# Kernel optimization log

Measured on AMD Instinct MI355X. Metric: run time of the kernel, lower is better.

## Reference

```python
import jax, jax.numpy as jnp
import numpy as np

FRACS = (0.25, 0.5, 0.25)  # per-expert top-fraction kept, from the original forward


def setup_inputs() -> dict:
    key = jax.random.key(0)
    ks = jax.random.split(key, 10)
    B, S, D, P, E, C = 1, 65536, 1024, 512, 3, 2
    s = 0.02
    return {
        "hidden_states": jax.random.normal(ks[0], (B, S, D), jnp.float32),
        "W_t1": jax.random.normal(ks[1], (D, P), jnp.float32) * s,   # TransMIL stand-in proj
        "W_cls1": jax.random.normal(ks[2], (P, C), jnp.float32) * s, # trans1 bag classifier
        "Wg0": jax.random.normal(ks[3], (P, 2), jnp.float32) * s,    # gate
        "Wg1": jax.random.normal(ks[4], (P, 2), jnp.float32) * s,    # gate1
        "Wg2": jax.random.normal(ks[5], (P, 2), jnp.float32) * s,    # gate2
        "W_clf": jax.random.normal(ks[6], (E, P, E), jnp.float32) * s,  # per-expert classifiers
        "W_a1": jax.random.normal(ks[7], (P, P), jnp.float32) * s,   # agg1 TransMIL stand-in proj
        "W_acls": jax.random.normal(ks[8], (P, C), jnp.float32) * s, # agg1 bag classifier
    }


def reference(hidden_states, W_t1, W_cls1, Wg0, Wg1, Wg2, W_clf, W_a1, W_acls):
    B, S, D = hidden_states.shape
    x = hidden_states.reshape(-1, D)               # (T, D) tokens
    T = x.shape[0]
    # trans1 (TransMIL stand-in): per-patch feature + mean-pool bag logits
    patches = jnp.tanh(x @ W_t1)                   # (T, P) patch_feature
    bag = patches.mean(0)
    Y_logits = (bag @ W_cls1)[None, :]             # (1, C)
    Y_prob = jax.nn.softmax(Y_logits, -1)
    Y_hat = jnp.argmax(Y_logits, -1)
    # three independent routers, softmax + top-1
    router_logits = patches @ Wg0                  # (T, 2)
    rw0 = jax.nn.softmax(router_logits.astype(jnp.float32), -1)
    w_top0 = rw0.max(-1)                           # top-1 routing weight (gate0) used as sort key for ALL experts
    sel0 = jnp.argmax(rw0, -1)
    sel1 = jnp.argmax(jax.nn.softmax((patches @ Wg1).astype(jnp.float32), -1), -1)
    sel2 = jnp.argmax(jax.nn.softmax((patches @ Wg2).astype(jnp.float32), -1), -1)
    masks = [sel0 == 1, sel1 == 1, sel2 == 1]      # expert_mask[e][1] token selection
    joint_losses = jnp.float32(0.0)
    sel_fs, nums_list = [], []
    for e in range(3):
        mask = masks[e]
        cnt = mask.sum().astype(jnp.int32)
        nums = jnp.floor(cnt.astype(jnp.float32) * FRACS[e]).astype(jnp.int32)
        nums = jnp.where(nums == 0, cnt, nums)     # 'if nums != 0 else all' branch
        key_ = jnp.where(mask, w_top0, -jnp.inf)
        order = jnp.argsort(-key_)                 # descending routing weight
        rank = jnp.zeros(T, jnp.int32).at[order].set(jnp.arange(T, dtype=jnp.int32))
        sel = mask & (rank < nums)                 # top-fraction tokens of this expert
        sel_f = sel.astype(patches.dtype)
        mean_feat = (patches * sel_f[:, None]).sum(0) / jnp.maximum(nums, 1).astype(patches.dtype)
        logits = mean_feat @ W_clf[e]              # (3,)
        if e < 2:                                  # CE loss only for experts 0,1
            joint_losses = joint_losses + (-jax.nn.log_softmax(logits)[e])
        sel_fs.append(sel_f)
        nums_list.append(nums)
    # agg1 (TransMIL stand-in) over concatenated represent_patchs == multiplicity-weighted mean
    feats2 = jnp.tanh(patches @ W_a1)              # (T, P)
    total_sel = sel_fs[0] + sel_fs[1] + sel_fs[2]
    total_n = (nums_list[0] + nums_list[1] + nums_list[2]).astype(patches.dtype)
    agg_bag = (feats2 * total_sel[:, None]).sum(0) / jnp.maximum(total_n, 1.0)
    e_Y_logits = (agg_bag @ W_acls)[None, :]
    e_Y_hat = jnp.argmax(e_Y_logits, -1)
    distribute = jnp.stack([jnp.asarray(T, jnp.int32), nums_list[0], nums_list[1], nums_list[2]])
    return (e_Y_logits, e_Y_hat, Y_logits, Y_prob, Y_hat, router_logits, joint_losses, distribute)
```

## Files before the change

kernel.cpp:

```cpp
#include <hip/hip_runtime.h>
#include <cstdint>
#include <cstddef>

#define T_TOK 65536
#define DDIM  1024
#define PDIM  512

typedef __attribute__((ext_vector_type(8))) short          shortx8;
typedef __attribute__((ext_vector_type(8))) unsigned short ushortx8;
typedef __attribute__((ext_vector_type(4))) float          floatx4;

__device__ __forceinline__ unsigned short f2bf_rn(float x){
  unsigned int u = __float_as_uint(x);
  unsigned int r = u + 0x7FFFu + ((u >> 16) & 1u);
  return (unsigned short)(r >> 16);
}
__device__ __forceinline__ float bf2f(unsigned short h){
  return __uint_as_float(((unsigned int)h) << 16);
}
__device__ __forceinline__ float ftanh(float x){
  float ez = __expf(2.f * x);
  return 1.f - 2.f / (ez + 1.f);
}

__device__ __forceinline__ void gload16(const void* g, void* l){
  __builtin_amdgcn_global_load_lds(
      (const __attribute__((address_space(1))) unsigned int*)g,
      (__attribute__((address_space(3))) unsigned int*)l, 16, 0, 0);
}
__device__ __forceinline__ void bar(){
  asm volatile("" ::: "memory");
  __builtin_amdgcn_s_barrier();
  asm volatile("" ::: "memory");
}
#define WAIT_VMC(n) asm volatile("s_waitcnt vmcnt(" #n ")" ::: "memory")
#define WAIT_LGKM0  do { asm volatile("s_waitcnt lgkmcnt(0)" ::: "memory"); \
                         __builtin_amdgcn_sched_barrier(0); } while(0)

__device__ __forceinline__ void split2(const float4 a, const float4 b,
                                       ushortx8* hi, ushortx8* lo){
  float vs[8] = {a.x, a.y, a.z, a.w, b.x, b.y, b.z, b.w};
  ushortx8 h, l;
  #pragma unroll
  for (int j = 0; j < 8; j++){
    unsigned int u = __float_as_uint(vs[j]);
    float r = vs[j] - __uint_as_float(u & 0xFFFF0000u);
    h[j] = (unsigned short)(u >> 16);
    l[j] = (unsigned short)(__float_as_uint(r) >> 16);
  }
  *hi = h; *lo = l;
}


__global__ void prep(const float* __restrict__ Wt1, const float* __restrict__ Wa1,
                     unsigned short* __restrict__ W1th, unsigned short* __restrict__ W1tl,
                     unsigned short* __restrict__ Wath, unsigned short* __restrict__ Watl,
                     int* __restrict__ zbase)
{
  int gid = blockIdx.x * 256 + threadIdx.x;
  if (gid < 20544){ zbase[gid] = 0; return; }
  int i = gid - 20544;
  if (i < 524288){
    int e   = i & 7;
    int g16 = i >> 3;
    int s   = g16 & 3;
    int row = (g16 >> 2) & 255;
    int tb  = g16 >> 10;
    int nb  = tb & 1, kt = tb >> 1;
    int n = nb * 256 + row;
    int k = kt * 32 + ((s ^ ((row >> 1) & 3)) << 3) + e;
    float x = Wt1[(size_t)k * PDIM + n];
    unsigned short h = f2bf_rn(x);
    W1th[i] = h;
    W1tl[i] = f2bf_rn(x - bf2f(h));
    return;
  }
  i -= 524288;
  if (i < 262144){
    int e   = i & 7;
    int g16 = i >> 3;
    int s   = g16 & 3;
    int row = (g16 >> 2) & 255;
    int tb  = g16 >> 10;
    int nb  = tb & 1, kt = tb >> 1;
    int n = nb * 256 + row;
    int k = kt * 32 + ((s ^ ((row >> 1) & 3)) << 3) + e;
    float x = Wa1[(size_t)k * PDIM + n];
    unsigned short h = f2bf_rn(x);
    Wath[i] = h;
    Watl[i] = f2bf_rn(x - bf2f(h));
  }
}

template<int MODE>
__global__ __launch_bounds__(512, 2)
void gemm_split(const float* __restrict__ A,
                const unsigned short* __restrict__ Bhg,
                const unsigned short* __restrict__ Blg,
                float* __restrict__ Cout,
                float* __restrict__ colacc,
                const int* __restrict__ cidx,
                const float* __restrict__ wgt,
                const int* __restrict__ params)
{
  constexpr int K  = (MODE == 0) ? 1024 : 512;
  constexpr int NT = K >> 5;

  __shared__ unsigned short AhL[2][8192];
  __shared__ unsigned short AlL[2][8192];
  __shared__ unsigned short BhL[2][8192];
  __shared__ unsigned short BlL[2][8192];
  __shared__ int   cidxl[256];
  __shared__ float wl[256];

  const int tid = threadIdx.x;
  const int d = blockIdx.x + (blockIdx.y << 1);
  const int lin = (MODE == 0) ? (((d & 7) << 6) + (d >> 3)) : d;
  const int bx = lin & 1, by = lin >> 1;
  const int m0 = by << 8, n0 = bx << 8;

  if (MODE == 1){
    const int count = params[21];
    if (m0 >= count) return;
    if (tid < 256){
      int g = m0 + tid;
      if (g < count){ cidxl[tid] = cidx[g]; wl[tid] = wgt[g]; }
      else          { cidxl[tid] = 0;       wl[tid] = 0.f;   }
    }
    __syncthreads();
  }

  const int lane = tid & 63;
  const int wv   = tid >> 6;
  const int wm   = wv >> 2;
  const int wn   = wv & 3;
  const int lr   = lane & 15, quad = lane >> 4;
  const int sq   = (quad ^ ((lr >> 1) & 3)) << 4;

  const int abase = (wm * 128 + lr) * 64 + sq;
  const int bbase = (wn * 64  + lr) * 64 + sq;

  const int rowW = tid >> 1, half = tid & 1;
  const size_t arowg = (MODE == 0) ? (size_t)(m0 + rowW) : (size_t)cidxl[rowW];
  const float* ap = A + arowg * K + half * 16;
  const int rsw = (rowW >> 1) & 3;
  const int wb0 = rowW * 64 + ((( half * 2     ) ^ rsw) << 4);
  const int wb1 = rowW * 64 + ((( half * 2 + 1 ) ^ rsw) << 4);

  floatx4 acc[8][4];
  #pragma unroll
  for (int i = 0; i < 8; i++)
    #pragma unroll
    for (int j = 0; j < 4; j++)
      acc[i][j] = (floatx4){0.f, 0.f, 0.f, 0.f};

  float4 av0, av1, av2, av3;

  {
    av0 = *(const float4*)(ap + 0);
    av1 = *(const float4*)(ap + 4);
    av2 = *(const float4*)(ap + 8);
    av3 = *(const float4*)(ap + 12);
    const size_t tb = (size_t)bx * 8192;
    gload16(Bhg + tb + tid * 8,        (char*)BhL[0] + tid * 16);
    gload16(Bhg + tb + 4096 + tid * 8, (char*)BhL[0] + 8192 + tid * 16);
    gload16(Blg + tb + tid * 8,        (char*)BlL[0] + tid * 16);
    gload16(Blg + tb + 4096 + tid * 8, (char*)BlL[0] + 8192 + tid * 16);
    WAIT_VMC(4);
    ushortx8 h, l;
    split2(av0, av1, &h, &l);
    *(ushortx8*)((char*)AhL[0] + wb0) = h;
    *(ushortx8*)((char*)AlL[0] + wb0) = l;
    split2(av2, av3, &h, &l);
    *(ushortx8*)((char*)AhL[0] + wb1) = h;
    *(ushortx8*)((char*)AlL[0] + wb1) = l;
    {
      const float* apk = ap + ((NT > 1) ? 32 : 0);
      av0 = *(const float4*)(apk);
      av1 = *(const float4*)(apk + 4);
      av2 = *(const float4*)(apk + 8);
      av3 = *(const float4*)(apk + 12);
    }
    WAIT_VMC(4);
    asm volatile("s_waitcnt lgkmcnt(0)" ::: "memory");
    bar();
  }

  #pragma unroll 2
  for (int t = 0; t < NT; ++t){
    const int cur = t & 1, nxt = cur ^ 1;
    const int knB = (t + 1 < NT) ? (t + 1) : (NT - 1);
    const int knA = (t + 2 < NT) ? (t + 2) : (NT - 1);
    const char* AhC = (const char*)AhL[cur];
    const char* AlC = (const char*)AlL[cur];
    const char* BhC = (const char*)BhL[cur];
    const char* BlC = (const char*)BlL[cur];

    shortx8 aH[4], aL[4], bH0[2], bL0[2], bH1[2], bL1[2];

    #pragma unroll
    for (int mt = 0; mt < 4; mt++){
      aH[mt] = *(const shortx8*)(AhC + abase + mt * 1024);
      aL[mt] = *(const shortx8*)(AlC + abase + mt * 1024);
    }
    #pragma unroll
    for (int nt = 0; nt < 2; nt++){
      bH0[nt] = *(const shortx8*)(BhC + bbase + nt * 1024);
      bL0[nt] = *(const shortx8*)(BlC + bbase + nt * 1024);
    }
    {
      const size_t tb = (size_t)(knB * 2 + bx) * 8192;
      gload16(Bhg + tb + tid * 8,        (char*)BhL[nxt] + tid * 16);
      gload16(Bhg + tb + 4096 + tid * 8, (char*)BhL[nxt] + 8192 + tid * 16);
      gload16(Blg + tb + tid * 8,        (char*)BlL[nxt] + tid * 16);
      gload16(Blg + tb + 4096 + tid * 8, (char*)BlL[nxt] + 8192 + tid * 16);
    }
    bar();
    WAIT_LGKM0;
    __builtin_amdgcn_s_setprio(1);
    #pragma unroll
    for (int mt = 0; mt < 4; mt++)
      #pragma unroll
      for (int nt = 0; nt < 2; nt++){
        acc[mt][nt] = __builtin_amdgcn_mfma_f32_16x16x32_bf16(aH[mt], bH0[nt], acc[mt][nt], 0, 0, 0);
        acc[mt][nt] = __builtin_amdgcn_mfma_f32_16x16x32_bf16(aL[mt], bH0[nt], acc[mt][nt], 0, 0, 0);
        acc[mt][nt] = __builtin_amdgcn_mfma_f32_16x16x32_bf16(aH[mt], bL0[nt], acc[mt][nt], 0, 0, 0);
      }
    __builtin_amdgcn_s_setprio(0);
    bar();

    #pragma unroll
    for (int nt = 0; nt < 2; nt++){
      bH1[nt] = *(const shortx8*)(BhC + bbase + (2 + nt) * 1024);
      bL1[nt] = *(const shortx8*)(BlC + bbase + (2 + nt) * 1024);
    }
    WAIT_VMC(4);
    {
      ushortx8 h, l;
      split2(av0, av1, &h, &l);
      *(ushortx8*)((char*)AhL[nxt] + wb0) = h;
      *(ushortx8*)((char*)AlL[nxt] + wb0) = l;
      split2(av2, av3, &h, &l);
      *(ushortx8*)((char*)AhL[nxt] + wb1) = h;
      *(ushortx8*)((char*)AlL[nxt] + wb1) = l;
    }
    bar();
    WAIT_LGKM0;
    __builtin_amdgcn_s_setprio(1);
    #pragma unroll
    for (int mt = 0; mt < 4; mt++)
      #pragma unroll
      for (int nt = 0; nt < 2; nt++){
        acc[mt][2 + nt] = __builtin_amdgcn_mfma_f32_16x16x32_bf16(aH[mt], bH1[nt], acc[mt][2 + nt], 0, 0, 0);
        acc[mt][2 + nt] = __builtin_amdgcn_mfma_f32_16x16x32_bf16(aL[mt], bH1[nt], acc[mt][2 + nt], 0, 0, 0);
        acc[mt][2 + nt] = __builtin_amdgcn_mfma_f32_16x16x32_bf16(aH[mt], bL1[nt], acc[mt][2 + nt], 0, 0, 0);
      }
    __builtin_amdgcn_s_setprio(0);
    bar();

    #pragma unroll
    for (int mt = 0; mt < 4; mt++){
      aH[mt] = *(const shortx8*)(AhC + abase + (4 + mt) * 1024);
      aL[mt] = *(const shortx8*)(AlC + abase + (4 + mt) * 1024);
    }
    {
      const float* apk = ap + knA * 32;
      av0 = *(const float4*)(apk);
      av1 = *(const float4*)(apk + 4);
      av2 = *(const float4*)(apk + 8);
      av3 = *(const float4*)(apk + 12);
    }
    bar();
    WAIT_LGKM0;
    __builtin_amdgcn_s_setprio(1);
    #pragma unroll
    for (int mt = 0; mt < 4; mt++)
      #pragma unroll
      for (int nt = 0; nt < 2; nt++){
        acc[4 + mt][nt] = __builtin_amdgcn_mfma_f32_16x16x32_bf16(aH[mt], bH0[nt], acc[4 + mt][nt], 0, 0, 0);
        acc[4 + mt][nt] = __builtin_amdgcn_mfma_f32_16x16x32_bf16(aL[mt], bH0[nt], acc[4 + mt][nt], 0, 0, 0);
        acc[4 + mt][nt] = __builtin_amdgcn_mfma_f32_16x16x32_bf16(aH[mt], bL0[nt], acc[4 + mt][nt], 0, 0, 0);
      }
    #pragma unroll
    for (int mt = 0; mt < 4; mt++)
      #pragma unroll
      for (int nt = 0; nt < 2; nt++){
        acc[4 + mt][2 + nt] = __builtin_amdgcn_mfma_f32_16x16x32_bf16(aH[mt], bH1[nt], acc[4 + mt][2 + nt], 0, 0, 0);
        acc[4 + mt][2 + nt] = __builtin_amdgcn_mfma_f32_16x16x32_bf16(aL[mt], bH1[nt], acc[4 + mt][2 + nt], 0, 0, 0);
        acc[4 + mt][2 + nt] = __builtin_amdgcn_mfma_f32_16x16x32_bf16(aH[mt], bL1[nt], acc[4 + mt][2 + nt], 0, 0, 0);
      }
    __builtin_amdgcn_s_setprio(0);
    WAIT_VMC(4);
    bar();
  }

  float csum[4] = {0.f, 0.f, 0.f, 0.f};
  #pragma unroll
  for (int mt = 0; mt < 8; mt++){
    float w0 = 1.f, w1 = 1.f, w2 = 1.f, w3 = 1.f;
    if (MODE == 1){
      const float4 wv4 = *(const float4*)&wl[wm * 128 + mt * 16 + (quad << 2)];
      w0 = wv4.x; w1 = wv4.y; w2 = wv4.z; w3 = wv4.w;
    }
    #pragma unroll
    for (int nt = 0; nt < 4; nt++){
      float t0 = ftanh(acc[mt][nt][0]);
      float t1 = ftanh(acc[mt][nt][1]);
      float t2 = ftanh(acc[mt][nt][2]);
      float t3 = ftanh(acc[mt][nt][3]);
      if (MODE == 0){
        size_t base = (size_t)(m0 + wm * 128 + mt * 16 + (quad << 2)) * PDIM
                    + (n0 + wn * 64 + nt * 16 + lr);
        Cout[base]            = t0;
        Cout[base +     PDIM] = t1;
        Cout[base + 2 * PDIM] = t2;
        Cout[base + 3 * PDIM] = t3;
        csum[nt] += t0 + t1 + t2 + t3;
      } else {
        csum[nt] += t0 * w0 + t1 * w1 + t2 * w2 + t3 * w3;
      }
    }
  }
  #pragma unroll
  for (int nt = 0; nt < 4; nt++){
    float s = csum[nt];
    s += __shfl_xor(s, 16);
    s += __shfl_xor(s, 32);
    if (lane < 16) atomicAdd(&colacc[n0 + wn * 64 + nt * 16 + lane], s);
  }
}

__global__ void gates_kernel(const float* __restrict__ patches,
                             const float* __restrict__ Wg0,
                             const float* __restrict__ Wg1,
                             const float* __restrict__ Wg2,
                             float* __restrict__ dout,
                             unsigned int* __restrict__ wkey,
                             unsigned char* __restrict__ mask3,
                             int* __restrict__ params,
                             int* __restrict__ hist)
{
  __shared__ int lc[3];
  const int tid = threadIdx.x;
  if (tid < 3) lc[tid] = 0;
  __syncthreads();
  const int lane = tid & 63;
  float wg[3][16];
  const float* Wgp[3] = {Wg0, Wg1, Wg2};
  #pragma unroll
  for (int g = 0; g < 3; g++){
    #pragma unroll
    for (int j = 0; j < 4; j++){
      float4 v = *(const float4*)(Wgp[g] + lane * 16 + j * 4);
      wg[g][j * 4 + 0] = v.x; wg[g][j * 4 + 1] = v.y;
      wg[g][j * 4 + 2] = v.z; wg[g][j * 4 + 3] = v.w;
    }
  }
  const int nw = gridDim.x << 2;
  for (int t = blockIdx.x * 4 + (tid >> 6); t < T_TOK; t += nw){
    const float* row = patches + (size_t)t * PDIM + lane * 8;
    float4 v0 = *(const float4*)row;
    float4 v1 = *(const float4*)(row + 4);
    float x[8] = {v0.x, v0.y, v0.z, v0.w, v1.x, v1.y, v1.z, v1.w};
    float g00 = 0, g01 = 0, g10 = 0, g11 = 0, g20 = 0, g21 = 0;
    #pragma unroll
    for (int j = 0; j < 8; j++){
      g00 += x[j] * wg[0][2 * j]; g01 += x[j] * wg[0][2 * j + 1];
      g10 += x[j] * wg[1][2 * j]; g11 += x[j] * wg[1][2 * j + 1];
      g20 += x[j] * wg[2][2 * j]; g21 += x[j] * wg[2][2 * j + 1];
    }
    #pragma unroll
    for (int off = 1; off < 64; off <<= 1){
      g00 += __shfl_xor(g00, off); g01 += __shfl_xor(g01, off);
      g10 += __shfl_xor(g10, off); g11 += __shfl_xor(g11, off);
      g20 += __shfl_xor(g20, off); g21 += __shfl_xor(g21, off);
    }
    if (lane == 0){
      dout[8 + 2 * t]     = g00;
      dout[8 + 2 * t + 1] = g01;
      int m0 = g01 > g00;
      int m1 = g11 > g10;
      int m2 = g21 > g20;
      mask3[t] = (unsigned char)(m0 | (m1 << 1) | (m2 << 2));
      float d = fabsf(g00 - g01);
      float w = 1.0f / (1.0f + __expf(-d));
      unsigned int u = __float_as_uint(w);
      u = u < 0x3F000000u ? 0x3F000000u : u;
      u = u > 0x3F7FFFFFu ? 0x3F7FFFFFu : u;
      wkey[t] = u;
      int b = (int)((u >> 11) & 0xFFFu);
      if (m0){ atomicAdd(&hist[b], 1);         atomicAdd(&lc[0], 1); }
      if (m1){ atomicAdd(&hist[4096 + b], 1);  atomicAdd(&lc[1], 1); }
      if (m2){ atomicAdd(&hist[8192 + b], 1);  atomicAdd(&lc[2], 1); }
    }
  }
  __syncthreads();
  if (tid < 3 && lc[tid]) atomicAdd(&params[tid], lc[tid]);
}

__global__ void find_bucket(int* __restrict__ params, const int* __restrict__ hist)
{
  __shared__ int cs[256], orig[256];
  __shared__ int selc, selrk;
  const int tid = threadIdx.x;
  for (int e = 0; e < 3; e++){
    int cnt = params[e];
    int shift = (e == 1) ? 1 : 2;
    int nums = cnt >> shift;
    if (nums == 0) nums = cnt;
    if (tid == 0) params[3 + e] = nums;
    __syncthreads();
    if (nums == 0){
      if (tid == 0){ params[6 + e] = -1; params[9 + e] = 0; }
      __syncthreads();
      continue;
    }
    const int* h = hist + e * 4096 + tid * 16;
    int s = 0;
    #pragma unroll
    for (int j = 0; j < 16; j++) s += h[j];
    cs[tid] = s; orig[tid] = s;
    __syncthreads();
    for (int off = 1; off < 256; off <<= 1){
      int v = (tid + off < 256) ? cs[tid + off] : 0;
      __syncthreads();
      cs[tid] += v;
      __syncthreads();
    }
    if (cs[tid] >= nums && (cs[tid] - orig[tid]) < nums){
      selc = tid; selrk = nums - (cs[tid] - orig[tid]);
    }
    __syncthreads();
    if (tid == 0){
      int ch = selc, rk = selrk;
      const int* hh = hist + e * 4096 + ch * 16;
      int acc = 0;
      for (int j = 15; j >= 0; j--){
        int c = hh[j];
        if (acc + c >= rk){ params[6 + e] = ch * 16 + j; params[9 + e] = rk - acc; break; }
        acc += c;
      }
    }
    __syncthreads();
  }
}

__global__ void level2hist(const int* __restrict__ params, const unsigned int* __restrict__ wkey,
                           const unsigned char* __restrict__ mask3, int* __restrict__ h2)
{
  const int e = blockIdx.y;
  const int B = params[6 + e];
  if (B < 0) return;
  const unsigned char bit = (unsigned char)(1u << e);
  const int t0 = blockIdx.x * 2048 + threadIdx.x;
  #pragma unroll
  for (int i = 0; i < 8; i++){
    int t = t0 + i * 256;
    if (mask3[t] & bit){
      unsigned int u = wkey[t];
      if ((int)((u >> 11) & 0xFFFu) == B) atomicAdd(&h2[e * 2048 + (u & 2047u)], 1);
    }
  }
}

__global__ void find_theta(int* __restrict__ params, const int* __restrict__ h2)
{
  const int e = blockIdx.x;
  const int tid = threadIdx.x;
  __shared__ int cs[256], orig[256];
  __shared__ int selc;
  int B = params[6 + e], rank = params[9 + e];
  if (B < 0){
    if (tid == 0){ params[12 + e] = (int)0xFFFFFFFFu; params[15 + e] = 0; params[18 + e] = 0; }
    return;
  }
  const int* h = h2 + e * 2048 + tid * 8;
  int s = 0;
  #pragma unroll
  for (int j = 0; j < 8; j++) s += h[j];
  cs[tid] = s; orig[tid] = s;
  __syncthreads();
  for (int off = 1; off < 256; off <<= 1){
    int v = (tid + off < 256) ? cs[tid + off] : 0;
    __syncthreads();
    cs[tid] += v;
    __syncthreads();
  }
  if (cs[tid] >= rank && (cs[tid] - orig[tid]) < rank) selc = tid;
  __syncthreads();
  if (tid == 0){
    int ch = selc;
    int rk = rank - (cs[ch] - orig[ch]);
    const int* hh = h2 + e * 2048 + ch * 8;
    int acc = 0;
    for (int j = 7; j >= 0; j--){
      int c = hh[j];
      if (acc + c >= rk){
        int sub = ch * 8 + j;
        params[12 + e] = (int)(0x3F000000u | ((unsigned)B << 11) | (unsigned)sub);
        params[15 + e] = rk - acc;
        params[18 + e] = c;
        break;
      }
      acc += c;
    }
  }
}

__global__ void mark_sel(const int* __restrict__ params, const unsigned int* __restrict__ wkey,
                         const unsigned char* __restrict__ mask3, unsigned char* __restrict__ selb)
{
  const int e = blockIdx.y;
  const int bx = blockIdx.x;
  const int tid = threadIdx.x;
  const unsigned int theta = (unsigned int)params[12 + e];
  const int r = params[15 + e];
  const int ceq = params[18 + e];
  const unsigned char bit = (unsigned char)(1u << e);
  unsigned char* sb = selb + e * T_TOK;
  if (ceq == r){
    int t0 = bx * 2048;
    #pragma unroll
    for (int i = 0; i < 8; i++){
      int t = t0 + i * 256 + tid;
      unsigned char mk = mask3[t] & bit;
      sb[t] = (mk && wkey[t] >= theta) ? 1 : 0;
    }
  } else {
    if (bx) return;
    __shared__ int basec;
    __shared__ int wsum[4];
    if (tid == 0) basec = 0;
    __syncthreads();
    const int lane = tid & 63, w = tid >> 6;
    for (int c = 0; c < 256; c++){
      int t = c * 256 + tid;
      unsigned char mk = mask3[t] & bit;
      unsigned int u = mk ? wkey[t] : 0u;
      bool gt = mk && (u > theta);
      bool eq = mk && (u == theta);
      unsigned long long bal = __ballot(eq);
      if (lane == 0) wsum[w] = __popcll(bal);
      __syncthreads();
      int wbase = 0;
      for (int ww = 0; ww < w; ww++) wbase += wsum[ww];
      int pos = basec + wbase + __popcll(bal & ((1ull << lane) - 1ull));
      sb[t] = (gt || (eq && pos < r)) ? 1 : 0;
      __syncthreads();
      if (tid == 0) basec += wsum[0] + wsum[1] + wsum[2] + wsum[3];
      __syncthreads();
    }
  }
}

__global__ void compact(const unsigned char* __restrict__ selb, int* __restrict__ cidx,
                        float* __restrict__ wgt, int* __restrict__ params)
{
  int t = blockIdx.x * 256 + threadIdx.x;
  int ts = selb[t] + selb[T_TOK + t] + selb[2 * T_TOK + t];
  int lane = threadIdx.x & 63;
  unsigned long long bal = __ballot(ts > 0);
  int base = 0;
  if (lane == 0) base = atomicAdd(&params[21], __popcll(bal));
  base = __shfl(base, 0);
  if (ts){
    int pos = base + __popcll(bal & ((1ull << lane) - 1ull));
    cidx[pos] = t;
    wgt[pos] = (float)ts;
  }
}

__global__ void meanfeat_c(const float* __restrict__ patches, const unsigned char* __restrict__ selb,
                           const int* __restrict__ cidx, const int* __restrict__ params,
                           float* __restrict__ mf)
{
  const int count = params[21];
  const int base = blockIdx.x * 256;
  if (base >= count) return;
  const int n = min(256, count - base);
  const int tid = threadIdx.x;
  __shared__ int cl[256];
  __shared__ unsigned char f0s[256], f1s[256];
  if (tid < n){
    int c = cidx[base + tid];
    cl[tid] = c;
    f0s[tid] = selb[c];
    f1s[tid] = selb[T_TOK + c];
  }
  __syncthreads();
  float s00 = 0, s01 = 0, s10 = 0, s11 = 0;
  for (int i = 0; i < n; i++){
    int f0 = f0s[i], f1 = f1s[i];
    if (f0 | f1){
      float2 v = *(const float2*)(patches + (size_t)cl[i] * PDIM + tid * 2);
      if (f0){ s00 += v.x; s01 += v.y; }
      if (f1){ s10 += v.x; s11 += v.y; }
    }
  }
  atomicAdd(&mf[tid * 2],       s00);
  atomicAdd(&mf[tid * 2 + 1],   s01);
  atomicAdd(&mf[512 + tid * 2],     s10);
  atomicAdd(&mf[512 + tid * 2 + 1], s11);
}

__global__ void finalize(const float* __restrict__ bagsum, const float* __restrict__ aggsum,
                         const float* __restrict__ mf, const int* __restrict__ params,
                         const float* __restrict__ Wcls1, const float* __restrict__ Wclf,
                         const float* __restrict__ Wacls, float* __restrict__ dout)
{
  const int lane = threadIdx.x;
  const int nums0 = params[3], nums1 = params[4], nums2 = params[5];
  const float invT = 1.0f / 65536.0f;
  const float inv0 = 1.0f / (float)(nums0 > 0 ? nums0 : 1);
  const float inv1 = 1.0f / (float)(nums1 > 0 ? nums1 : 1);
  const float totn = (float)(nums0 + nums1 + nums2);
  const float invA = 1.0f / fmaxf(totn, 1.0f);
  float y0 = 0, y1 = 0, a0 = 0, a1 = 0;
  float l00 = 0, l01 = 0, l02 = 0, l10 = 0, l11 = 0, l12 = 0;
  #pragma unroll
  for (int j = 0; j < 8; j++){
    int p = lane * 8 + j;
    float bg = bagsum[p] * invT;
    y0 += bg * Wcls1[p * 2]; y1 += bg * Wcls1[p * 2 + 1];
    float ag = aggsum[p] * invA;
    a0 += ag * Wacls[p * 2]; a1 += ag * Wacls[p * 2 + 1];
    float m0v = mf[p] * inv0;
    l00 += m0v * Wclf[p * 3]; l01 += m0v * Wclf[p * 3 + 1]; l02 += m0v * Wclf[p * 3 + 2];
    float m1v = mf[512 + p] * inv1;
    l10 += m1v * Wclf[1536 + p * 3]; l11 += m1v * Wclf[1536 + p * 3 + 1]; l12 += m1v * Wclf[1536 + p * 3 + 2];
  }
  #pragma unroll
  for (int off = 1; off < 64; off <<= 1){
    y0 += __shfl_xor(y0, off);   y1 += __shfl_xor(y1, off);
    a0 += __shfl_xor(a0, off);   a1 += __shfl_xor(a1, off);
    l00 += __shfl_xor(l00, off); l01 += __shfl_xor(l01, off); l02 += __shfl_xor(l02, off);
    l10 += __shfl_xor(l10, off); l11 += __shfl_xor(l11, off); l12 += __shfl_xor(l12, off);
  }
  if (lane == 0){
    dout[0] = a0; dout[1] = a1;
    dout[2] = (a1 > a0) ? 1.0f : 0.0f;
    dout[3] = y0; dout[4] = y1;
    float mx = fmaxf(y0, y1), e0 = expf(y0 - mx), e1 = expf(y1 - mx), inv = 1.0f / (e0 + e1);
    dout[5] = e0 * inv; dout[6] = e1 * inv;
    dout[7] = (y1 > y0) ? 1.0f : 0.0f;
    float m3 = fmaxf(fmaxf(l00, l01), l02);
    float lse0 = m3 + logf(expf(l00 - m3) + expf(l01 - m3) + expf(l02 - m3));
    float m4 = fmaxf(fmaxf(l10, l11), l12);
    float lse1 = m4 + logf(expf(l10 - m4) + expf(l11 - m4) + expf(l12 - m4));
    dout[131080] = (lse0 - l00) + (lse1 - l11);
    dout[131081] = 65536.0f;
    dout[131082] = (float)nums0;
    dout[131083] = (float)nums1;
    dout[131084] = (float)nums2;
  }
}

extern "C" void kernel_launch(void* const* d_in, const int* in_sizes, int n_in,
                              void* d_out, int out_size, void* d_ws, size_t ws_size,
                              hipStream_t stream)
{
  const float* X      = (const float*)d_in[0];
  const float* W_t1   = (const float*)d_in[1];
  const float* W_cls1 = (const float*)d_in[2];
  const float* Wg0    = (const float*)d_in[3];
  const float* Wg1    = (const float*)d_in[4];
  const float* Wg2    = (const float*)d_in[5];
  const float* W_clf  = (const float*)d_in[6];
  const float* W_a1   = (const float*)d_in[7];
  const float* W_acls = (const float*)d_in[8];
  float* dout = (float*)d_out;
  char* ws = (char*)d_ws;

  float*          patches = (float*)         (ws + 0);
  unsigned short* W1th    = (unsigned short*)(ws + 134217728);
  unsigned short* W1tl    = (unsigned short*)(ws + 135266304);
  unsigned short* Wath    = (unsigned short*)(ws + 136314880);
  unsigned short* Watl    = (unsigned short*)(ws + 136839168);
  unsigned int*   wkey    = (unsigned int*)  (ws + 137363456);
  unsigned char*  mask3   = (unsigned char*) (ws + 137625600);
  unsigned char*  selb    = (unsigned char*) (ws + 137691136);
  int*            cidx    = (int*)           (ws + 137887744);
  float*          wgt     = (float*)         (ws + 138149888);
  int*            zbase   = (int*)           (ws + 138412032);
  int*            hist    = zbase;
  int*            h2      = zbase + 12288;
  int*            params  = zbase + 18432;
  float*          bagsum  = (float*)(zbase + 18496);
  float*          aggsum  = (float*)(zbase + 19008);
  float*          mf      = (float*)(zbase + 19520);

  prep<<<3153, 256, 0, stream>>>(W_t1, W_a1, W1th, W1tl, Wath, Watl, zbase);

  gemm_split<0><<<dim3(2, 256), 512, 0, stream>>>(
      X, W1th, W1tl, patches, bagsum, nullptr, nullptr, nullptr);

  gates_kernel<<<512, 256, 0, stream>>>(
      patches, Wg0, Wg1, Wg2, dout, wkey, mask3, params, hist);

  find_bucket<<<1, 256, 0, stream>>>(params, hist);
  level2hist<<<dim3(32, 3), 256, 0, stream>>>(params, wkey, mask3, h2);
  find_theta<<<3, 256, 0, stream>>>(params, h2);
  mark_sel<<<dim3(32, 3), 256, 0, stream>>>(params, wkey, mask3, selb);
  compact<<<256, 256, 0, stream>>>(selb, cidx, wgt, params);

  meanfeat_c<<<256, 256, 0, stream>>>(patches, selb, cidx, params, mf);

  gemm_split<1><<<dim3(2, 256), 512, 0, stream>>>(
      patches, Wath, Watl, nullptr, aggsum, cidx, wgt, params);

  finalize<<<1, 64, 0, stream>>>(bagsum, aggsum, mf, params, W_cls1, W_clf, W_acls, dout);
}
```

Baseline: 726.6 us.

## Split GEMM main loop into eight 2x2 MFMA phases with finer LDS interleaving

Restructures the inner k-loop from four large MFMA clusters into eight smaller 2x2-subtile phases, in a serpentine order that reuses A/B fragment registers across phases. LDS reads and global prefetches are interleaved between the smaller clusters. The aim is to lower register pressure and overlap LDS traffic with MFMA work. The cost is many more barriers per iteration, which may add sync overhead.

```diff
diff --git a/kernel.cpp b/kernel.cpp
--- a/kernel.cpp
+++ b/kernel.cpp
@@ -49,6 +49,23 @@
     l[j] = (unsigned short)(__float_as_uint(r) >> 16);
   }
   *hi = h; *lo = l;
+}
+
+template<int P, int Q>
+__device__ __forceinline__ void mfma12(floatx4 (&acc)[8][4],
+    const shortx8 aH[2], const shortx8 aL[2],
+    const shortx8 bH[2], const shortx8 bL[2])
+{
+  #pragma unroll
+  for (int i = 0; i < 2; i++)
+    #pragma unroll
+    for (int j = 0; j < 2; j++){
+      floatx4 c = acc[2*P+i][2*Q+j];
+      c = __builtin_amdgcn_mfma_f32_16x16x32_bf16(aH[i], bH[j], c, 0, 0, 0);
+      c = __builtin_amdgcn_mfma_f32_16x16x32_bf16(aL[i], bH[j], c, 0, 0, 0);
+      c = __builtin_amdgcn_mfma_f32_16x16x32_bf16(aH[i], bL[j], c, 0, 0, 0);
+      acc[2*P+i][2*Q+j] = c;
+    }
 }
 
 
@@ -195,74 +212,83 @@
     const char* AlC = (const char*)AlL[cur];
     const char* BhC = (const char*)BhL[cur];
     const char* BlC = (const char*)BlL[cur];
-
-    shortx8 aH[4], aL[4], bH0[2], bL0[2], bH1[2], bL1[2];
-
-    #pragma unroll
-    for (int mt = 0; mt < 4; mt++){
-      aH[mt] = *(const shortx8*)(AhC + abase + mt * 1024);
-      aL[mt] = *(const shortx8*)(AlC + abase + mt * 1024);
-    }
-    #pragma unroll
-    for (int nt = 0; nt < 2; nt++){
-      bH0[nt] = *(const shortx8*)(BhC + bbase + nt * 1024);
-      bL0[nt] = *(const shortx8*)(BlC + bbase + nt * 1024);
+    char* AhN = (char*)AhL[nxt];
+    char* AlN = (char*)AlL[nxt];
+    char* BhN = (char*)BhL[nxt];
+    char* BlN = (char*)BlL[nxt];
+
+    shortx8 aXH[2], aXL[2], aYH[2], aYL[2];
+    shortx8 b0H[2], b0L[2], b1H[2], b1L[2];
+
+    #pragma unroll
+    for (int i = 0; i < 2; i++){
+      aXH[i] = *(const shortx8*)(AhC + abase + i * 1024);
+      aXL[i] = *(const shortx8*)(AlC + abase + i * 1024);
+      b0H[i] = *(const shortx8*)(BhC + bbase + i * 1024);
+      b0L[i] = *(const shortx8*)(BlC + bbase + i * 1024);
     }
     {
       const size_t tb = (size_t)(knB * 2 + bx) * 8192;
-      gload16(Bhg + tb + tid * 8,        (char*)BhL[nxt] + tid * 16);
-      gload16(Bhg + tb + 4096 + tid * 8, (char*)BhL[nxt] + 8192 + tid * 16);
-      gload16(Blg + tb + tid * 8,        (char*)BlL[nxt] + tid * 16);
-      gload16(Blg + tb + 4096 + tid * 8, (char*)BlL[nxt] + 8192 + tid * 16);
-    }
-    bar();
-    WAIT_LGKM0;
+      gload16(Bhg + tb + tid * 8,        BhN + tid * 16);
+      gload16(Bhg + tb + 4096 + tid * 8, BhN + 8192 + tid * 16);
+      gload16(Blg + tb + tid * 8,        BlN + tid * 16);
+      gload16(Blg + tb + 4096 + tid * 8, BlN + 8192 + tid * 16);
+    }
+    bar(); WAIT_LGKM0;
     __builtin_amdgcn_s_setprio(1);
-    #pragma unroll
-    for (int mt = 0; mt < 4; mt++)
-      #pragma unroll
-      for (int nt = 0; nt < 2; nt++){
-        acc[mt][nt] = __builtin_amdgcn_mfma_f32_16x16x32_bf16(aH[mt], bH0[nt], acc[mt][nt], 0, 0, 0);
-        acc[mt][nt] = __builtin_amdgcn_mfma_f32_16x16x32_bf16(aL[mt], bH0[nt], acc[mt][nt], 0, 0, 0);
-        acc[mt][nt] = __builtin_amdgcn_mfma_f32_16x16x32_bf16(aH[mt], bL0[nt], acc[mt][nt], 0, 0, 0);
-      }
+    mfma12<0,0>(acc, aXH, aXL, b0H, b0L);
     __builtin_amdgcn_s_setprio(0);
     bar();
 
     #pragma unroll
-    for (int nt = 0; nt < 2; nt++){
-      bH1[nt] = *(const shortx8*)(BhC + bbase + (2 + nt) * 1024);
-      bL1[nt] = *(const shortx8*)(BlC + bbase + (2 + nt) * 1024);
+    for (int j = 0; j < 2; j++){
+      b1H[j] = *(const shortx8*)(BhC + bbase + (2 + j) * 1024);
+      b1L[j] = *(const shortx8*)(BlC + bbase + (2 + j) * 1024);
+    }
+    bar(); WAIT_LGKM0;
+    __builtin_amdgcn_s_setprio(1);
+    mfma12<0,1>(acc, aXH, aXL, b1H, b1L);
+    __builtin_amdgcn_s_setprio(0);
+    bar();
+
+    #pragma unroll
+    for (int i = 0; i < 2; i++){
+      aYH[i] = *(const shortx8*)(AhC + abase + (2 + i) * 1024);
+      aYL[i] = *(const shortx8*)(AlC + abase + (2 + i) * 1024);
     }
     WAIT_VMC(4);
     {
       ushortx8 h, l;
       split2(av0, av1, &h, &l);
-      *(ushortx8*)((char*)AhL[nxt] + wb0) = h;
-      *(ushortx8*)((char*)AlL[nxt] + wb0) = l;
+      *(ushortx8*)(AhN + wb0) = h;
+      *(ushortx8*)(AlN + wb0) = l;
       split2(av2, av3, &h, &l);
-      *(ushortx8*)((char*)AhL[nxt] + wb1) = h;
-      *(ushortx8*)((char*)AlL[nxt] + wb1) = l;
-    }
-    bar();
-    WAIT_LGKM0;
+      *(ushortx8*)(AhN + wb1) = h;
+      *(ushortx8*)(AlN + wb1) = l;
+    }
+    bar(); WAIT_LGKM0;
     __builtin_amdgcn_s_setprio(1);
-    #pragma unroll
-    for (int mt = 0; mt < 4; mt++)
-      #pragma unroll
-      for (int nt = 0; nt < 2; nt++){
-        acc[mt][2 + nt] = __builtin_amdgcn_mfma_f32_16x16x32_bf16(aH[mt], bH1[nt], acc[mt][2 + nt], 0, 0, 0);
-        acc[mt][2 + nt] = __builtin_amdgcn_mfma_f32_16x16x32_bf16(aL[mt], bH1[nt], acc[mt][2 + nt], 0, 0, 0);
-        acc[mt][2 + nt] = __builtin_amdgcn_mfma_f32_16x16x32_bf16(aH[mt], bL1[nt], acc[mt][2 + nt], 0, 0, 0);
-      }
+    mfma12<1,1>(acc, aYH, aYL, b1H, b1L);
     __builtin_amdgcn_s_setprio(0);
     bar();
 
-    #pragma unroll
-    for (int mt = 0; mt < 4; mt++){
-      aH[mt] = *(const shortx8*)(AhC + abase + (4 + mt) * 1024);
-      aL[mt] = *(const shortx8*)(AlC + abase + (4 + mt) * 1024);
-    }
+    bar(); WAIT_LGKM0;
+    __builtin_amdgcn_s_setprio(1);
+    mfma12<1,0>(acc, aYH, aYL, b0H, b0L);
+    __builtin_amdgcn_s_setprio(0);
+    bar();
+
+    #pragma unroll
+    for (int i = 0; i < 2; i++){
+      aXH[i] = *(const shortx8*)(AhC + abase + (4 + i) * 1024);
+      aXL[i] = *(const shortx8*)(AlC + abase + (4 + i) * 1024);
+    }
+    bar(); WAIT_LGKM0;
+    __builtin_amdgcn_s_setprio(1);
+    mfma12<2,0>(acc, aXH, aXL, b0H, b0L);
+    __builtin_amdgcn_s_setprio(0);
+    bar();
+
     {
       const float* apk = ap + knA * 32;
       av0 = *(const float4*)(apk);
@@ -270,25 +296,26 @@
       av2 = *(const float4*)(apk + 8);
       av3 = *(const float4*)(apk + 12);
     }
-    bar();
-    WAIT_LGKM0;
+    bar(); WAIT_LGKM0;
     __builtin_amdgcn_s_setprio(1);
-    #pragma unroll
-    for (int mt = 0; mt < 4; mt++)
-      #pragma unroll
-      for (int nt = 0; nt < 2; nt++){
-        acc[4 + mt][nt] = __builtin_amdgcn_mfma_f32_16x16x32_bf16(aH[mt], bH0[nt], acc[4 + mt][nt], 0, 0, 0);
-        acc[4 + mt][nt] = __builtin_amdgcn_mfma_f32_16x16x32_bf16(aL[mt], bH0[nt], acc[4 + mt][nt], 0, 0, 0);
-        acc[4 + mt][nt] = __builtin_amdgcn_mfma_f32_16x16x32_bf16(aH[mt], bL0[nt], acc[4 + mt][nt], 0, 0, 0);
-      }
-    #pragma unroll
-    for (int mt = 0; mt < 4; mt++)
-      #pragma unroll
-      for (int nt = 0; nt < 2; nt++){
-        acc[4 + mt][2 + nt] = __builtin_amdgcn_mfma_f32_16x16x32_bf16(aH[mt], bH1[nt], acc[4 + mt][2 + nt], 0, 0, 0);
-        acc[4 + mt][2 + nt] = __builtin_amdgcn_mfma_f32_16x16x32_bf16(aL[mt], bH1[nt], acc[4 + mt][2 + nt], 0, 0, 0);
-        acc[4 + mt][2 + nt] = __builtin_amdgcn_mfma_f32_16x16x32_bf16(aH[mt], bL1[nt], acc[4 + mt][2 + nt], 0, 0, 0);
-      }
+    mfma12<2,1>(acc, aXH, aXL, b1H, b1L);
+    __builtin_amdgcn_s_setprio(0);
+    bar();
+
+    #pragma unroll
+    for (int i = 0; i < 2; i++){
+      aYH[i] = *(const shortx8*)(AhC + abase + (6 + i) * 1024);
+      aYL[i] = *(const shortx8*)(AlC + abase + (6 + i) * 1024);
+    }
+    bar(); WAIT_LGKM0;
+    __builtin_amdgcn_s_setprio(1);
+    mfma12<3,1>(acc, aYH, aYL, b1H, b1L);
+    __builtin_amdgcn_s_setprio(0);
+    bar();
+
+    bar(); WAIT_LGKM0;
+    __builtin_amdgcn_s_setprio(1);
+    mfma12<3,0>(acc, aYH, aYL, b0H, b0L);
     __builtin_amdgcn_s_setprio(0);
     WAIT_VMC(4);
     bar();
```

Result: slower. 774.4 us (+6.6%).

## Shrink split-bf16 GEMM tiles from 256x256 to 128x128 with 256-thread blocks

Applied to the files above, without the earlier changes.

Reduces the gemm_split block tile from 256x256 (8 waves) to 128x128 (4 waves), halving LDS buffers and accumulator registers, and drops two of the four MFMA phases per k-step. The weight pre-swizzle in prep is changed to match the 128-wide N blocks, and the grid grows to 4x512 blocks. The aim is more resident blocks per CU and better load balance, especially for the variable-count MODE 1 pass. The cost is lower operand reuse per tile, so A and B traffic from global memory rises.

```diff
diff --git a/kernel.cpp b/kernel.cpp
--- a/kernel.cpp
+++ b/kernel.cpp
@@ -64,10 +64,10 @@
     int e   = i & 7;
     int g16 = i >> 3;
     int s   = g16 & 3;
-    int row = (g16 >> 2) & 255;
-    int tb  = g16 >> 10;
-    int nb  = tb & 1, kt = tb >> 1;
-    int n = nb * 256 + row;
+    int row = (g16 >> 2) & 127;
+    int tb  = g16 >> 9;
+    int nb  = tb & 3, kt = tb >> 2;
+    int n = nb * 128 + row;
     int k = kt * 32 + ((s ^ ((row >> 1) & 3)) << 3) + e;
     float x = Wt1[(size_t)k * PDIM + n];
     unsigned short h = f2bf_rn(x);
@@ -80,10 +80,10 @@
     int e   = i & 7;
     int g16 = i >> 3;
     int s   = g16 & 3;
-    int row = (g16 >> 2) & 255;
-    int tb  = g16 >> 10;
-    int nb  = tb & 1, kt = tb >> 1;
-    int n = nb * 256 + row;
+    int row = (g16 >> 2) & 127;
+    int tb  = g16 >> 9;
+    int nb  = tb & 3, kt = tb >> 2;
+    int n = nb * 128 + row;
     int k = kt * 32 + ((s ^ ((row >> 1) & 3)) << 3) + e;
     float x = Wa1[(size_t)k * PDIM + n];
     unsigned short h = f2bf_rn(x);
@@ -93,7 +93,7 @@
 }
 
 template<int MODE>
-__global__ __launch_bounds__(512, 2)
+__global__ __launch_bounds__(256, 2)
 void gemm_split(const float* __restrict__ A,
                 const unsigned short* __restrict__ Bhg,
                 const unsigned short* __restrict__ Blg,
@@ -106,23 +106,23 @@
   constexpr int K  = (MODE == 0) ? 1024 : 512;
   constexpr int NT = K >> 5;
 
-  __shared__ unsigned short AhL[2][8192];
-  __shared__ unsigned short AlL[2][8192];
-  __shared__ unsigned short BhL[2][8192];
-  __shared__ unsigned short BlL[2][8192];
-  __shared__ int   cidxl[256];
-  __shared__ float wl[256];
+  __shared__ unsigned short AhL[2][4096];
+  __shared__ unsigned short AlL[2][4096];
+  __shared__ unsigned short BhL[2][4096];
+  __shared__ unsigned short BlL[2][4096];
+  __shared__ int   cidxl[128];
+  __shared__ float wl[128];
 
   const int tid = threadIdx.x;
-  const int d = blockIdx.x + (blockIdx.y << 1);
-  const int lin = (MODE == 0) ? (((d & 7) << 6) + (d >> 3)) : d;
-  const int bx = lin & 1, by = lin >> 1;
-  const int m0 = by << 8, n0 = bx << 8;
+  const int d = blockIdx.x + (blockIdx.y << 2);
+  const int lin = (MODE == 0) ? (((d & 7) << 8) + (d >> 3)) : d;
+  const int bx = lin & 3, by = lin >> 2;
+  const int m0 = by << 7, n0 = bx << 7;
 
   if (MODE == 1){
     const int count = params[21];
     if (m0 >= count) return;
-    if (tid < 256){
+    if (tid < 128){
       int g = m0 + tid;
       if (g < count){ cidxl[tid] = cidx[g]; wl[tid] = wgt[g]; }
       else          { cidxl[tid] = 0;       wl[tid] = 0.f;   }
@@ -132,13 +132,13 @@
 
   const int lane = tid & 63;
   const int wv   = tid >> 6;
-  const int wm   = wv >> 2;
-  const int wn   = wv & 3;
+  const int wm   = wv >> 1;
+  const int wn   = wv & 1;
   const int lr   = lane & 15, quad = lane >> 4;
   const int sq   = (quad ^ ((lr >> 1) & 3)) << 4;
 
-  const int abase = (wm * 128 + lr) * 64 + sq;
-  const int bbase = (wn * 64  + lr) * 64 + sq;
+  const int abase = (wm * 64 + lr) * 64 + sq;
+  const int bbase = (wn * 64 + lr) * 64 + sq;
 
   const int rowW = tid >> 1, half = tid & 1;
   const size_t arowg = (MODE == 0) ? (size_t)(m0 + rowW) : (size_t)cidxl[rowW];
@@ -147,9 +147,9 @@
   const int wb0 = rowW * 64 + ((( half * 2     ) ^ rsw) << 4);
   const int wb1 = rowW * 64 + ((( half * 2 + 1 ) ^ rsw) << 4);
 
-  floatx4 acc[8][4];
-  #pragma unroll
-  for (int i = 0; i < 8; i++)
+  floatx4 acc[4][4];
+  #pragma unroll
+  for (int i = 0; i < 4; i++)
     #pragma unroll
     for (int j = 0; j < 4; j++)
       acc[i][j] = (floatx4){0.f, 0.f, 0.f, 0.f};
@@ -161,11 +161,11 @@
     av1 = *(const float4*)(ap + 4);
     av2 = *(const float4*)(ap + 8);
     av3 = *(const float4*)(ap + 12);
-    const size_t tb = (size_t)bx * 8192;
+    const size_t tb = (size_t)bx * 4096;
     gload16(Bhg + tb + tid * 8,        (char*)BhL[0] + tid * 16);
-    gload16(Bhg + tb + 4096 + tid * 8, (char*)BhL[0] + 8192 + tid * 16);
+    gload16(Bhg + tb + 2048 + tid * 8, (char*)BhL[0] + 4096 + tid * 16);
     gload16(Blg + tb + tid * 8,        (char*)BlL[0] + tid * 16);
-    gload16(Blg + tb + 4096 + tid * 8, (char*)BlL[0] + 8192 + tid * 16);
+    gload16(Blg + tb + 2048 + tid * 8, (char*)BlL[0] + 4096 + tid * 16);
     WAIT_VMC(4);
     ushortx8 h, l;
     split2(av0, av1, &h, &l);
@@ -195,8 +195,12 @@
     const char* AlC = (const char*)AlL[cur];
     const char* BhC = (const char*)BhL[cur];
     const char* BlC = (const char*)BlL[cur];
-
-    shortx8 aH[4], aL[4], bH0[2], bL0[2], bH1[2], bL1[2];
+    char* AhN = (char*)AhL[nxt];
+    char* AlN = (char*)AlL[nxt];
+    char* BhN = (char*)BhL[nxt];
+    char* BlN = (char*)BlL[nxt];
+
+    shortx8 aH[4], aL[4], b0H[2], b0L[2], b1H[2], b1L[2];
 
     #pragma unroll
     for (int mt = 0; mt < 4; mt++){
@@ -205,63 +209,43 @@
     }
     #pragma unroll
     for (int nt = 0; nt < 2; nt++){
-      bH0[nt] = *(const shortx8*)(BhC + bbase + nt * 1024);
-      bL0[nt] = *(const shortx8*)(BlC + bbase + nt * 1024);
+      b0H[nt] = *(const shortx8*)(BhC + bbase + nt * 1024);
+      b0L[nt] = *(const shortx8*)(BlC + bbase + nt * 1024);
     }
     {
-      const size_t tb = (size_t)(knB * 2 + bx) * 8192;
-      gload16(Bhg + tb + tid * 8,        (char*)BhL[nxt] + tid * 16);
-      gload16(Bhg + tb + 4096 + tid * 8, (char*)BhL[nxt] + 8192 + tid * 16);
-      gload16(Blg + tb + tid * 8,        (char*)BlL[nxt] + tid * 16);
-      gload16(Blg + tb + 4096 + tid * 8, (char*)BlL[nxt] + 8192 + tid * 16);
-    }
-    bar();
-    WAIT_LGKM0;
+      const size_t tb = (size_t)(knB * 4 + bx) * 4096;
+      gload16(Bhg + tb + tid * 8,        BhN + tid * 16);
+      gload16(Bhg + tb + 2048 + tid * 8, BhN + 4096 + tid * 16);
+      gload16(Blg + tb + tid * 8,        BlN + tid * 16);
+      gload16(Blg + tb + 2048 + tid * 8, BlN + 4096 + tid * 16);
+    }
+    bar(); WAIT_LGKM0;
     __builtin_amdgcn_s_setprio(1);
     #pragma unroll
     for (int mt = 0; mt < 4; mt++)
       #pragma unroll
       for (int nt = 0; nt < 2; nt++){
-        acc[mt][nt] = __builtin_amdgcn_mfma_f32_16x16x32_bf16(aH[mt], bH0[nt], acc[mt][nt], 0, 0, 0);
-        acc[mt][nt] = __builtin_amdgcn_mfma_f32_16x16x32_bf16(aL[mt], bH0[nt], acc[mt][nt], 0, 0, 0);
-        acc[mt][nt] = __builtin_amdgcn_mfma_f32_16x16x32_bf16(aH[mt], bL0[nt], acc[mt][nt], 0, 0, 0);
+        acc[mt][nt] = __builtin_amdgcn_mfma_f32_16x16x32_bf16(aH[mt], b0H[nt], acc[mt][nt], 0, 0, 0);
+        acc[mt][nt] = __builtin_amdgcn_mfma_f32_16x16x32_bf16(aL[mt], b0H[nt], acc[mt][nt], 0, 0, 0);
+        acc[mt][nt] = __builtin_amdgcn_mfma_f32_16x16x32_bf16(aH[mt], b0L[nt], acc[mt][nt], 0, 0, 0);
       }
     __builtin_amdgcn_s_setprio(0);
     bar();
 
     #pragma unroll
     for (int nt = 0; nt < 2; nt++){
-      bH1[nt] = *(const shortx8*)(BhC + bbase + (2 + nt) * 1024);
-      bL1[nt] = *(const shortx8*)(BlC + bbase + (2 + nt) * 1024);
+      b1H[nt] = *(const shortx8*)(BhC + bbase + (2 + nt) * 1024);
+      b1L[nt] = *(const shortx8*)(BlC + bbase + (2 + nt) * 1024);
     }
     WAIT_VMC(4);
     {
       ushortx8 h, l;
       split2(av0, av1, &h, &l);
-      *(ushortx8*)((char*)AhL[nxt] + wb0) = h;
-      *(ushortx8*)((char*)AlL[nxt] + wb0) = l;
+      *(ushortx8*)(AhN + wb0) = h;
+      *(ushortx8*)(AlN + wb0) = l;
       split2(av2, av3, &h, &l);
-      *(ushortx8*)((char*)AhL[nxt] + wb1) = h;
-      *(ushortx8*)((char*)AlL[nxt] + wb1) = l;
-    }
-    bar();
-    WAIT_LGKM0;
-    __builtin_amdgcn_s_setprio(1);
-    #pragma unroll
-    for (int mt = 0; mt < 4; mt++)
-      #pragma unroll
-      for (int nt = 0; nt < 2; nt++){
-        acc[mt][2 + nt] = __builtin_amdgcn_mfma_f32_16x16x32_bf16(aH[mt], bH1[nt], acc[mt][2 + nt], 0, 0, 0);
-        acc[mt][2 + nt] = __builtin_amdgcn_mfma_f32_16x16x32_bf16(aL[mt], bH1[nt], acc[mt][2 + nt], 0, 0, 0);
-        acc[mt][2 + nt] = __builtin_amdgcn_mfma_f32_16x16x32_bf16(aH[mt], bL1[nt], acc[mt][2 + nt], 0, 0, 0);
-      }
-    __builtin_amdgcn_s_setprio(0);
-    bar();
-
-    #pragma unroll
-    for (int mt = 0; mt < 4; mt++){
-      aH[mt] = *(const shortx8*)(AhC + abase + (4 + mt) * 1024);
-      aL[mt] = *(const shortx8*)(AlC + abase + (4 + mt) * 1024);
+      *(ushortx8*)(AhN + wb1) = h;
+      *(ushortx8*)(AlN + wb1) = l;
     }
     {
       const float* apk = ap + knA * 32;
@@ -270,24 +254,15 @@
       av2 = *(const float4*)(apk + 8);
       av3 = *(const float4*)(apk + 12);
     }
-    bar();
-    WAIT_LGKM0;
+    bar(); WAIT_LGKM0;
     __builtin_amdgcn_s_setprio(1);
     #pragma unroll
     for (int mt = 0; mt < 4; mt++)
       #pragma unroll
       for (int nt = 0; nt < 2; nt++){
-        acc[4 + mt][nt] = __builtin_amdgcn_mfma_f32_16x16x32_bf16(aH[mt], bH0[nt], acc[4 + mt][nt], 0, 0, 0);
-        acc[4 + mt][nt] = __builtin_amdgcn_mfma_f32_16x16x32_bf16(aL[mt], bH0[nt], acc[4 + mt][nt], 0, 0, 0);
-        acc[4 + mt][nt] = __builtin_amdgcn_mfma_f32_16x16x32_bf16(aH[mt], bL0[nt], acc[4 + mt][nt], 0, 0, 0);
-      }
-    #pragma unroll
-    for (int mt = 0; mt < 4; mt++)
-      #pragma unroll
-      for (int nt = 0; nt < 2; nt++){
-        acc[4 + mt][2 + nt] = __builtin_amdgcn_mfma_f32_16x16x32_bf16(aH[mt], bH1[nt], acc[4 + mt][2 + nt], 0, 0, 0);
-        acc[4 + mt][2 + nt] = __builtin_amdgcn_mfma_f32_16x16x32_bf16(aL[mt], bH1[nt], acc[4 + mt][2 + nt], 0, 0, 0);
-        acc[4 + mt][2 + nt] = __builtin_amdgcn_mfma_f32_16x16x32_bf16(aH[mt], bL1[nt], acc[4 + mt][2 + nt], 0, 0, 0);
+        acc[mt][2 + nt] = __builtin_amdgcn_mfma_f32_16x16x32_bf16(aH[mt], b1H[nt], acc[mt][2 + nt], 0, 0, 0);
+        acc[mt][2 + nt] = __builtin_amdgcn_mfma_f32_16x16x32_bf16(aL[mt], b1H[nt], acc[mt][2 + nt], 0, 0, 0);
+        acc[mt][2 + nt] = __builtin_amdgcn_mfma_f32_16x16x32_bf16(aH[mt], b1L[nt], acc[mt][2 + nt], 0, 0, 0);
       }
     __builtin_amdgcn_s_setprio(0);
     WAIT_VMC(4);
@@ -296,10 +271,10 @@
 
   float csum[4] = {0.f, 0.f, 0.f, 0.f};
   #pragma unroll
-  for (int mt = 0; mt < 8; mt++){
+  for (int mt = 0; mt < 4; mt++){
     float w0 = 1.f, w1 = 1.f, w2 = 1.f, w3 = 1.f;
     if (MODE == 1){
-      const float4 wv4 = *(const float4*)&wl[wm * 128 + mt * 16 + (quad << 2)];
+      const float4 wv4 = *(const float4*)&wl[wm * 64 + mt * 16 + (quad << 2)];
       w0 = wv4.x; w1 = wv4.y; w2 = wv4.z; w3 = wv4.w;
     }
     #pragma unroll
@@ -309,7 +284,7 @@
       float t2 = ftanh(acc[mt][nt][2]);
       float t3 = ftanh(acc[mt][nt][3]);
       if (MODE == 0){
-        size_t base = (size_t)(m0 + wm * 128 + mt * 16 + (quad << 2)) * PDIM
+        size_t base = (size_t)(m0 + wm * 64 + mt * 16 + (quad << 2)) * PDIM
                     + (n0 + wn * 64 + nt * 16 + lr);
         Cout[base]            = t0;
         Cout[base +     PDIM] = t1;
@@ -691,7 +666,7 @@
 
   prep<<<3153, 256, 0, stream>>>(W_t1, W_a1, W1th, W1tl, Wath, Watl, zbase);
 
-  gemm_split<0><<<dim3(2, 256), 512, 0, stream>>>(
+  gemm_split<0><<<dim3(4, 512), 256, 0, stream>>>(
       X, W1th, W1tl, patches, bagsum, nullptr, nullptr, nullptr);
 
   gates_kernel<<<512, 256, 0, stream>>>(
@@ -705,7 +680,7 @@
 
   meanfeat_c<<<256, 256, 0, stream>>>(patches, selb, cidx, params, mf);
 
-  gemm_split<1><<<dim3(2, 256), 512, 0, stream>>>(
+  gemm_split<1><<<dim3(4, 512), 256, 0, stream>>>(
       patches, Wath, Watl, nullptr, aggsum, cidx, wgt, params);
 
   finalize<<<1, 64, 0, stream>>>(bagsum, aggsum, mf, params, W_cls1, W_clf, W_acls, dout);
```

After: 733.6 us. About the same (+1.0%).
